# Performance work log

Hardware: AMD Instinct MI355X
Metric: run time of the kernel (lower is better)

The kernel has to match this reference:

```python
import jax, jax.numpy as jnp
import numpy as np

B, T, E, H = 8, 1024, 128, 8
S = E // H  # 16, narrow per-head dim


def setup_inputs() -> dict:
    key = jax.random.key(0)
    ks = jax.random.split(key, 7)
    return {
        "x": jax.random.normal(ks[0], (B, T, E), dtype=jnp.float32),
        "masks": jax.random.randint(ks[1], (B, T), 0, 2, dtype=jnp.int32),
        "Wq": jax.random.normal(ks[2], (S, S), dtype=jnp.float32) * 0.05,
        "Wk": jax.random.normal(ks[3], (S, S), dtype=jnp.float32) * 0.05,
        "Wv": jax.random.normal(ks[4], (S, S), dtype=jnp.float32) * 0.05,
        "Wu": jax.random.normal(ks[5], (E, E), dtype=jnp.float32) * 0.05,
        "bu": jnp.zeros((E,), dtype=jnp.float32),
        "temporal_only": 1,
    }


def reference(x, masks, Wq, Wk, Wv, Wu, bu, temporal_only):
    b, t, e = x.shape
    h = H
    s = e // h
    x4 = x.reshape(b, t, h, s)
    # nn.Linear(s, s, bias=False): y = x @ W.T, applied per head
    q = jnp.einsum('bths,ds->bthd', x4, Wq)
    k = jnp.einsum('bths,ds->bthd', x4, Wk)
    v = jnp.einsum('bths,ds->bthd', x4, Wv)
    scale = jnp.float32(e) ** 0.25
    q = q / scale
    k = k / scale
    # (b, h, t, t) attention logits
    dot = jnp.einsum('bqhd,bkhd->bhqk', q, k)
    # temporal_only masking: masks is (b, t), applied on key axis then query axis
    m = masks.astype(bool)
    neg = jnp.float32(-1e9)
    dot = jnp.where(m[:, None, None, :], dot, neg)
    dot = jnp.where(m[:, None, :, None], dot, neg)
    attn = jax.nn.softmax(dot, axis=-1)
    # post-softmax zeroing with the same masks
    attn = jnp.where(m[:, None, None, :], attn, jnp.float32(0.0))
    attn = jnp.where(m[:, None, :, None], attn, jnp.float32(0.0))
    out = jnp.einsum('bhqk,bkhd->bqhd', attn, v).reshape(b, t, h * s)
    return out @ Wu.T + bu
```

## Files before the change

### kernel.cpp

```cpp
#include <hip/hip_runtime.h>

#define NB 8
#define NT 1024
#define NE 128
#define NH 8
#define NS 16

#define WS_Q 0
#define WS_KC 1048576
#define WS_VC 2097152
#define WS_Y 3145728
#define WS_L 4194304
#define WS_VCNT (4194304 + 65536)

#define WT_PITCH 132

typedef float v2f __attribute__((ext_vector_type(2)));

static __device__ __forceinline__ v2f vlo(const float4 v) { return v2f{v.x, v.y}; }
static __device__ __forceinline__ v2f vhi(const float4 v) { return v2f{v.z, v.w}; }
static __device__ __forceinline__ v2f pfma(v2f a, v2f b, v2f c) {
  return __builtin_elementwise_fma(a, b, c);
}

static __device__ __forceinline__ float fexp2(float x) {
  return __builtin_amdgcn_exp2f(x);
}

static __device__ __forceinline__ void fma4(float4& acc, float s, const float4 v) {
  v2f lo = pfma(v2f{s, s}, vlo(v), vlo(acc));
  v2f hi = pfma(v2f{s, s}, vhi(v), vhi(acc));
  acc.x = lo.x; acc.y = lo.y; acc.z = hi.x; acc.w = hi.y;
}

static __device__ __forceinline__ float dot16p(const float4 q0, const float4 q1,
                                               const float4 q2, const float4 q3,
                                               const float4 k0, const float4 k1,
                                               const float4 k2, const float4 k3) {
  v2f a = vlo(q0) * vlo(k0);
  v2f b = vhi(q0) * vhi(k0);
  a = pfma(vlo(q1), vlo(k1), a);
  b = pfma(vhi(q1), vhi(k1), b);
  a = pfma(vlo(q2), vlo(k2), a);
  b = pfma(vhi(q2), vhi(k2), b);
  a = pfma(vlo(q3), vlo(k3), a);
  b = pfma(vhi(q3), vhi(k3), b);
  v2f c = a + b;
  return c.x + c.y;
}

__global__ __launch_bounds__(256) void qkv_kernel(
    const float* __restrict__ x, const int* __restrict__ masks,
    const float* __restrict__ Wq, const float* __restrict__ Wk,
    const float* __restrict__ Wv, float* __restrict__ Q,
    float* __restrict__ Kc, float* __restrict__ Vc, float* __restrict__ Y,
    float* __restrict__ L, int* __restrict__ vcount) {
  __shared__ __align__(16) float xs[64 * 20];
  __shared__ int posl[64];
  const int tid = threadIdx.x;
  const int h = blockIdx.x & 7;
  const int rg = blockIdx.x >> 3;
  const int b = rg >> 4;
  const int bt = (rg & 15) << 6;
  {
    const int sr = tid >> 2, sq = tid & 3;
    float4 xv =
        *(const float4*)(x + (size_t)(b * NT + bt + sr) * 128 + h * 16 + sq * 4);
    *(float4*)(xs + sr * 20 + sq * 4) = xv;
    *(float4*)(Y + (size_t)(b * NT + bt + sr) * NE + h * NS + sq * 4) =
        float4{0, 0, 0, 0};
  }
  if (tid < 64) {
    L[(size_t)(b * NH + h) * NT + bt + tid] = 0.f;
    int cnt = 0;
    for (int c = 0; c < bt; c += 64)
      cnt += __popcll(__ballot(masks[b * NT + c + tid] != 0));
    int v = masks[b * NT + bt + tid] != 0;
    unsigned long long bal = __ballot(v);
    posl[tid] = v ? (cnt + __popcll(bal & ((1ull << tid) - 1ull))) : -1;
    if (bt == NT - 64 && tid == 0) vcount[b] = cnt + __popcll(bal);
  }
  const int d = tid & 15;
  const int r = (tid >> 4) << 2;
  const float4* wq4 = (const float4*)(Wq + d * 16);
  const float4 wq0 = wq4[0], wq1 = wq4[1], wq2 = wq4[2], wq3 = wq4[3];
  const float4* wk4 = (const float4*)(Wk + d * 16);
  const float4 wk0 = wk4[0], wk1 = wk4[1], wk2 = wk4[2], wk3 = wk4[3];
  const float4* wv4 = (const float4*)(Wv + d * 16);
  const float4 wv0 = wv4[0], wv1 = wv4[1], wv2 = wv4[2], wv3 = wv4[3];
  const float invs = 0.12751744448143132f;
  __syncthreads();
#pragma unroll
  for (int i = 0; i < 4; i++) {
    const int row = r + i;
    const float4* xp = (const float4*)(xs + row * 20);
    const float4 x0 = xp[0], x1 = xp[1], x2 = xp[2], x3 = xp[3];
    float aq = dot16p(x0, x1, x2, x3, wq0, wq1, wq2, wq3);
    float ak = dot16p(x0, x1, x2, x3, wk0, wk1, wk2, wk3);
    float av = dot16p(x0, x1, x2, x3, wv0, wv1, wv2, wv3);
    const int t = bt + row;
    Q[((size_t)(b * NH + h) * NT + t) * NS + d] = aq * invs;
    const int pp = posl[row];
    if (pp >= 0) {
      size_t oc = ((size_t)(b * NH + h) * NT + pp) * NS + d;
      Kc[oc] = ak;
      Vc[oc] = av;
    }
  }
}

__global__ __launch_bounds__(512, 2) void attn_kernel(
    const float* __restrict__ Q, const float* __restrict__ Kc,
    const float* __restrict__ Vc, const int* __restrict__ vcount,
    float* __restrict__ Y, float* __restrict__ L) {
  __shared__ __align__(16) float smem[8192];
  float* Ks = smem;
  float* Vs = smem + 4096;
  const int tid = threadIdx.x;
  const int lane = tid & 63;
  const int s = tid >> 6;
  const int kh = blockIdx.x >> 8;
  const int rest = blockIdx.x & 255;
  const int bh = rest & 63;
  const int qg = rest >> 6;
  const int b = bh >> 3, h = bh & 7;
  const int tbase = qg << 8;
  const int nv = vcount[b];
  const int h0 = nv >> 1;
  const int kstart = kh ? h0 : 0;
  const int kend = kh ? nv : h0;

  float4 q[4][4];
#pragma unroll
  for (int qq = 0; qq < 4; qq++) {
    const float4* qg4 =
        (const float4*)(Q + ((size_t)bh * NT + tbase + (qq << 6) + lane) * NS);
    q[qq][0] = qg4[0]; q[qq][1] = qg4[1]; q[qq][2] = qg4[2]; q[qq][3] = qg4[3];
  }
  v2f o[4][8];
  float l[4];
#pragma unroll
  for (int qq = 0; qq < 4; qq++) {
    l[qq] = 0.f;
#pragma unroll
    for (int k = 0; k < 8; k++) o[qq][k] = v2f{0.f, 0.f};
  }

  const int quad = tid & 3;
  const int jr = tid >> 2;

#pragma unroll 1
  for (int k0 = kstart; k0 < kend; k0 += 256) {
    const int chunk = (kend - k0 < 256) ? (kend - k0) : 256;
    __syncthreads();
#pragma unroll
    for (int p = 0; p < 2; p++) {
      const int row = jr + (p << 7);
      float4 kv = {0, 0, 0, 0};
      if (row < chunk)
        kv = *(const float4*)(Kc + ((size_t)bh * NT + (k0 + row)) * NS +
                              (quad << 2));
      *(float4*)(Ks + row * 16 + (quad << 2)) = kv;
    }
#pragma unroll
    for (int p = 0; p < 2; p++) {
      const int row = jr + (p << 7);
      float4 vv = {0, 0, 0, 0};
      if (row < chunk)
        vv = *(const float4*)(Vc + ((size_t)bh * NT + (k0 + row)) * NS +
                              (quad << 2));
      *(float4*)(Vs + row * 16 + (quad << 2)) = vv;
    }
    __syncthreads();
#pragma unroll 2
    for (int g = 0; g < 8; g++) {
      const int rb = s + (g << 5);
      if (rb >= chunk) break;
      float sc[4][4];
#pragma unroll
      for (int i = 0; i < 4; i++) {
        const float4* kr = (const float4*)(Ks + (rb + (i << 3)) * 16);
        const float4 k0v = kr[0], k1v = kr[1], k2v = kr[2], k3v = kr[3];
#pragma unroll
        for (int qq = 0; qq < 4; qq++)
          sc[qq][i] =
              dot16p(q[qq][0], q[qq][1], q[qq][2], q[qq][3], k0v, k1v, k2v, k3v);
      }
#pragma unroll
      for (int i = 0; i < 4; i++)
        if (rb + (i << 3) >= chunk) {
          sc[0][i] = -1e30f; sc[1][i] = -1e30f;
          sc[2][i] = -1e30f; sc[3][i] = -1e30f;
        }
      float p[4][4];
#pragma unroll
      for (int qq = 0; qq < 4; qq++) {
        p[qq][0] = fexp2(sc[qq][0]);
        p[qq][1] = fexp2(sc[qq][1]);
        p[qq][2] = fexp2(sc[qq][2]);
        p[qq][3] = fexp2(sc[qq][3]);
        l[qq] += (p[qq][0] + p[qq][1]) + (p[qq][2] + p[qq][3]);
      }
#pragma unroll
      for (int i = 0; i < 4; i++) {
        const float4* vr = (const float4*)(Vs + (rb + (i << 3)) * 16);
        const float4 v0 = vr[0], v1 = vr[1], v2 = vr[2], v3 = vr[3];
#pragma unroll
        for (int qq = 0; qq < 4; qq++) {
          const v2f pq = {p[qq][i], p[qq][i]};
          o[qq][0] = pfma(pq, vlo(v0), o[qq][0]);
          o[qq][1] = pfma(pq, vhi(v0), o[qq][1]);
          o[qq][2] = pfma(pq, vlo(v1), o[qq][2]);
          o[qq][3] = pfma(pq, vhi(v1), o[qq][3]);
          o[qq][4] = pfma(pq, vlo(v2), o[qq][4]);
          o[qq][5] = pfma(pq, vhi(v2), o[qq][5]);
          o[qq][6] = pfma(pq, vlo(v3), o[qq][6]);
          o[qq][7] = pfma(pq, vhi(v3), o[qq][7]);
        }
      }
    }
  }

  float* om = smem;
  const int q8 = tid >> 3;
  const int sub = tid & 7;
#pragma unroll
  for (int ph = 0; ph < 4; ph++) {
    v2f ysum = {0.f, 0.f};
    float Lsum = 0.f;
    __syncthreads();
    if (s < 4) {
      float* pa = om + (s * 64 + lane) * 20;
#pragma unroll
      for (int k = 0; k < 8; k++) *(v2f*)(pa + k * 2) = o[ph][k];
      pa[16] = l[ph];
    }
    __syncthreads();
#pragma unroll
    for (int ss = 0; ss < 4; ss++) {
      const float* pp = om + (ss * 64 + q8) * 20;
      Lsum += pp[16];
      ysum += *(const v2f*)(pp + sub * 2);
    }
    __syncthreads();
    if (s >= 4) {
      float* pa = om + ((s - 4) * 64 + lane) * 20;
#pragma unroll
      for (int k = 0; k < 8; k++) *(v2f*)(pa + k * 2) = o[ph][k];
      pa[16] = l[ph];
    }
    __syncthreads();
#pragma unroll
    for (int ss = 0; ss < 4; ss++) {
      const float* pp = om + (ss * 64 + q8) * 20;
      Lsum += pp[16];
      ysum += *(const v2f*)(pp + sub * 2);
    }
    const int tq = tbase + (ph << 6) + q8;
    float* yp = Y + ((size_t)b * NT + tq) * NE + h * NS + sub * 2;
    atomicAdd(yp + 0, ysum.x);
    atomicAdd(yp + 1, ysum.y);
    if (sub == 0) atomicAdd(L + (size_t)bh * NT + tq, Lsum);
  }
}

__global__ __launch_bounds__(256) void proj_kernel(
    const float* __restrict__ Y, const float* __restrict__ L,
    const int* __restrict__ masks, const float* __restrict__ Wu,
    const float* __restrict__ bu, float* __restrict__ out) {
  __shared__ __align__(16) float Wt[64 * WT_PITCH];
  __shared__ __align__(16) float Yt[16 * 128];
  const int tid = threadIdx.x;
  const int r0 = blockIdx.x * 16;
  const int bb = r0 >> 10;
  const float4* yg = (const float4*)(Y + (size_t)r0 * 128);
  float4* yt4 = (float4*)Yt;
  {
#pragma unroll
    for (int p = 0; p < 2; p++) {
      const int idx = tid + p * 256;
      const int row = idx >> 5;
      const int head = (idx & 31) >> 2;
      const int t = (r0 + row) & 1023;
      const float Lv = L[(size_t)(bb * NH + head) * NT + t];
      const int qm = masks[r0 + row];
      const float inv = (qm != 0 && Lv > 0.f) ? (1.0f / Lv) : 0.f;
      float4 v = yg[idx];
      v.x *= inv; v.y *= inv; v.z *= inv; v.w *= inv;
      yt4[idx] = v;
    }
  }
  const int c0 = (tid & 31) << 2;
  const int rg = (tid >> 5) & 3;
  const int eh = tid >> 7;
  float4 acc0 = {0, 0, 0, 0}, acc1 = {0, 0, 0, 0}, acc2 = {0, 0, 0, 0},
         acc3 = {0, 0, 0, 0};
  for (int e0 = 0; e0 < 128; e0 += 64) {
    __syncthreads();
#pragma unroll
    for (int p = 0; p < 8; p++) {
      int idx = tid + p * 256;
      int c = idx >> 4;
      int es = (idx & 15) << 2;
      float4 w = *(const float4*)(Wu + c * 128 + e0 + es);
      Wt[(es + 0) * WT_PITCH + c] = w.x;
      Wt[(es + 1) * WT_PITCH + c] = w.y;
      Wt[(es + 2) * WT_PITCH + c] = w.z;
      Wt[(es + 3) * WT_PITCH + c] = w.w;
    }
    __syncthreads();
    const int eb = eh << 5;
    const float* y0 = Yt + (rg * 4 + 0) * 128 + e0 + eb;
    const float* y1 = Yt + (rg * 4 + 1) * 128 + e0 + eb;
    const float* y2 = Yt + (rg * 4 + 2) * 128 + e0 + eb;
    const float* y3 = Yt + (rg * 4 + 3) * 128 + e0 + eb;
#pragma unroll 4
    for (int e = 0; e < 32; e += 4) {
      const float* wb = Wt + (eb + e) * WT_PITCH + c0;
      float4 w0 = *(const float4*)(wb + 0 * WT_PITCH);
      float4 w1 = *(const float4*)(wb + 1 * WT_PITCH);
      float4 w2 = *(const float4*)(wb + 2 * WT_PITCH);
      float4 w3 = *(const float4*)(wb + 3 * WT_PITCH);
      float4 ya = *(const float4*)(y0 + e);
      float4 yb = *(const float4*)(y1 + e);
      float4 yc = *(const float4*)(y2 + e);
      float4 yd = *(const float4*)(y3 + e);
      fma4(acc0, ya.x, w0); fma4(acc0, ya.y, w1); fma4(acc0, ya.z, w2); fma4(acc0, ya.w, w3);
      fma4(acc1, yb.x, w0); fma4(acc1, yb.y, w1); fma4(acc1, yb.z, w2); fma4(acc1, yb.w, w3);
      fma4(acc2, yc.x, w0); fma4(acc2, yc.y, w1); fma4(acc2, yc.z, w2); fma4(acc2, yc.w, w3);
      fma4(acc3, yd.x, w0); fma4(acc3, yd.y, w1); fma4(acc3, yd.z, w2); fma4(acc3, yd.w, w3);
    }
  }
  __syncthreads();
  if (eh == 1) {
    float* p = Wt + (tid & 127) * 20;
    *(float4*)(p + 0) = acc0; *(float4*)(p + 4) = acc1;
    *(float4*)(p + 8) = acc2; *(float4*)(p + 12) = acc3;
  }
  __syncthreads();
  if (eh == 0) {
    const float* p = Wt + tid * 20;
    float4 b4 = *(const float4*)(bu + c0);
    float4 q0 = *(const float4*)(p + 0);
    float4 q1 = *(const float4*)(p + 4);
    float4 q2 = *(const float4*)(p + 8);
    float4 q3 = *(const float4*)(p + 12);
    acc0.x += q0.x + b4.x; acc0.y += q0.y + b4.y; acc0.z += q0.z + b4.z; acc0.w += q0.w + b4.w;
    acc1.x += q1.x + b4.x; acc1.y += q1.y + b4.y; acc1.z += q1.z + b4.z; acc1.w += q1.w + b4.w;
    acc2.x += q2.x + b4.x; acc2.y += q2.y + b4.y; acc2.z += q2.z + b4.z; acc2.w += q2.w + b4.w;
    acc3.x += q3.x + b4.x; acc3.y += q3.y + b4.y; acc3.z += q3.z + b4.z; acc3.w += q3.w + b4.w;
    *(float4*)(out + (size_t)(r0 + rg * 4 + 0) * 128 + c0) = acc0;
    *(float4*)(out + (size_t)(r0 + rg * 4 + 1) * 128 + c0) = acc1;
    *(float4*)(out + (size_t)(r0 + rg * 4 + 2) * 128 + c0) = acc2;
    *(float4*)(out + (size_t)(r0 + rg * 4 + 3) * 128 + c0) = acc3;
  }
}

extern "C" void kernel_launch(void* const* d_in, const int* in_sizes, int n_in,
                              void* d_out, int out_size, void* d_ws,
                              size_t ws_size, hipStream_t stream) {
  const float* x = (const float*)d_in[0];
  const int* masks = (const int*)d_in[1];
  const float* Wq = (const float*)d_in[2];
  const float* Wk = (const float*)d_in[3];
  const float* Wv = (const float*)d_in[4];
  const float* Wu = (const float*)d_in[5];
  const float* bu = (const float*)d_in[6];
  float* out = (float*)d_out;

  float* ws = (float*)d_ws;
  float* Q = ws + WS_Q;
  float* Kc = ws + WS_KC;
  float* Vc = ws + WS_VC;
  float* Y = ws + WS_Y;
  float* L = ws + WS_L;
  int* vcount = (int*)(ws + WS_VCNT);

  qkv_kernel<<<1024, 256, 0, stream>>>(x, masks, Wq, Wk, Wv, Q, Kc, Vc, Y, L,
                                       vcount);
  attn_kernel<<<2 * 4 * NB * NH, 512, 0, stream>>>(Q, Kc, Vc, vcount, Y, L);
  proj_kernel<<<NB * NT / 16, 256, 0, stream>>>(Y, L, masks, Wu, bu, out);
}
```

Before: 136.7 us.

## Replace atomic split-K accumulation with per-half partial buffers summed in projection

Each of the two key-split attention blocks now writes its partial output and row-sum into its own buffer with plain stores, and the projection kernel adds the two halves before normalising. This removes the float atomics, the zero-initialisation of Y and L in the QKV kernel, and two of the four barriers per phase in the in-block reduction, since all eight waves now write to a larger shared buffer at once. In exchange it uses more workspace, more shared memory per block (40 KB instead of 32 KB), and an extra global read of the second buffer in the projection kernel.

```diff
diff --git a/kernel.cpp b/kernel.cpp
--- a/kernel.cpp
+++ b/kernel.cpp
@@ -9,9 +9,11 @@
 #define WS_Q 0
 #define WS_KC 1048576
 #define WS_VC 2097152
-#define WS_Y 3145728
-#define WS_L 4194304
-#define WS_VCNT (4194304 + 65536)
+#define WS_Y0 3145728
+#define WS_Y1 4194304
+#define WS_L0 5242880
+#define WS_L1 (5242880 + 65536)
+#define WS_VCNT (5242880 + 131072)
 
 #define WT_PITCH 132
 
@@ -53,8 +55,7 @@
     const float* __restrict__ x, const int* __restrict__ masks,
     const float* __restrict__ Wq, const float* __restrict__ Wk,
     const float* __restrict__ Wv, float* __restrict__ Q,
-    float* __restrict__ Kc, float* __restrict__ Vc, float* __restrict__ Y,
-    float* __restrict__ L, int* __restrict__ vcount) {
+    float* __restrict__ Kc, float* __restrict__ Vc, int* __restrict__ vcount) {
   __shared__ __align__(16) float xs[64 * 20];
   __shared__ int posl[64];
   const int tid = threadIdx.x;
@@ -67,11 +68,8 @@
     float4 xv =
         *(const float4*)(x + (size_t)(b * NT + bt + sr) * 128 + h * 16 + sq * 4);
     *(float4*)(xs + sr * 20 + sq * 4) = xv;
-    *(float4*)(Y + (size_t)(b * NT + bt + sr) * NE + h * NS + sq * 4) =
-        float4{0, 0, 0, 0};
   }
   if (tid < 64) {
-    L[(size_t)(b * NH + h) * NT + bt + tid] = 0.f;
     int cnt = 0;
     for (int c = 0; c < bt; c += 64)
       cnt += __popcll(__ballot(masks[b * NT + c + tid] != 0));
@@ -112,8 +110,9 @@
 __global__ __launch_bounds__(512, 2) void attn_kernel(
     const float* __restrict__ Q, const float* __restrict__ Kc,
     const float* __restrict__ Vc, const int* __restrict__ vcount,
-    float* __restrict__ Y, float* __restrict__ L) {
-  __shared__ __align__(16) float smem[8192];
+    float* __restrict__ Y0, float* __restrict__ Y1, float* __restrict__ L0,
+    float* __restrict__ L1) {
+  __shared__ __align__(16) float smem[10240];
   float* Ks = smem;
   float* Vs = smem + 4096;
   const int tid = threadIdx.x;
@@ -129,6 +128,8 @@
   const int h0 = nv >> 1;
   const int kstart = kh ? h0 : 0;
   const int kend = kh ? nv : h0;
+  float* Yh = kh ? Y1 : Y0;
+  float* Lh = kh ? L1 : L0;
 
   float4 q[4][4];
 #pragma unroll
@@ -226,46 +227,33 @@
   const int sub = tid & 7;
 #pragma unroll
   for (int ph = 0; ph < 4; ph++) {
-    v2f ysum = {0.f, 0.f};
-    float Lsum = 0.f;
-    __syncthreads();
-    if (s < 4) {
+    __syncthreads();
+    {
       float* pa = om + (s * 64 + lane) * 20;
 #pragma unroll
       for (int k = 0; k < 8; k++) *(v2f*)(pa + k * 2) = o[ph][k];
       pa[16] = l[ph];
     }
     __syncthreads();
-#pragma unroll
-    for (int ss = 0; ss < 4; ss++) {
-      const float* pp = om + (ss * 64 + q8) * 20;
-      Lsum += pp[16];
-      ysum += *(const v2f*)(pp + sub * 2);
-    }
-    __syncthreads();
-    if (s >= 4) {
-      float* pa = om + ((s - 4) * 64 + lane) * 20;
-#pragma unroll
-      for (int k = 0; k < 8; k++) *(v2f*)(pa + k * 2) = o[ph][k];
-      pa[16] = l[ph];
-    }
-    __syncthreads();
-#pragma unroll
-    for (int ss = 0; ss < 4; ss++) {
-      const float* pp = om + (ss * 64 + q8) * 20;
-      Lsum += pp[16];
-      ysum += *(const v2f*)(pp + sub * 2);
-    }
-    const int tq = tbase + (ph << 6) + q8;
-    float* yp = Y + ((size_t)b * NT + tq) * NE + h * NS + sub * 2;
-    atomicAdd(yp + 0, ysum.x);
-    atomicAdd(yp + 1, ysum.y);
-    if (sub == 0) atomicAdd(L + (size_t)bh * NT + tq, Lsum);
+    {
+      float Lsum = 0.f;
+      v2f ysum = {0.f, 0.f};
+#pragma unroll
+      for (int ss = 0; ss < 8; ss++) {
+        const float* pp = om + (ss * 64 + q8) * 20;
+        Lsum += pp[16];
+        ysum += *(const v2f*)(pp + sub * 2);
+      }
+      const int tq = tbase + (ph << 6) + q8;
+      *(v2f*)(Yh + ((size_t)b * NT + tq) * NE + h * NS + sub * 2) = ysum;
+      if (sub == 0) Lh[(size_t)bh * NT + tq] = Lsum;
+    }
   }
 }
 
 __global__ __launch_bounds__(256) void proj_kernel(
-    const float* __restrict__ Y, const float* __restrict__ L,
+    const float* __restrict__ Y0, const float* __restrict__ Y1,
+    const float* __restrict__ L0, const float* __restrict__ L1,
     const int* __restrict__ masks, const float* __restrict__ Wu,
     const float* __restrict__ bu, float* __restrict__ out) {
   __shared__ __align__(16) float Wt[64 * WT_PITCH];
@@ -273,7 +261,8 @@
   const int tid = threadIdx.x;
   const int r0 = blockIdx.x * 16;
   const int bb = r0 >> 10;
-  const float4* yg = (const float4*)(Y + (size_t)r0 * 128);
+  const float4* yg0 = (const float4*)(Y0 + (size_t)r0 * 128);
+  const float4* yg1 = (const float4*)(Y1 + (size_t)r0 * 128);
   float4* yt4 = (float4*)Yt;
   {
 #pragma unroll
@@ -282,12 +271,15 @@
       const int row = idx >> 5;
       const int head = (idx & 31) >> 2;
       const int t = (r0 + row) & 1023;
-      const float Lv = L[(size_t)(bb * NH + head) * NT + t];
+      const size_t li = (size_t)(bb * NH + head) * NT + t;
+      const float Lv = L0[li] + L1[li];
       const int qm = masks[r0 + row];
       const float inv = (qm != 0 && Lv > 0.f) ? (1.0f / Lv) : 0.f;
-      float4 v = yg[idx];
-      v.x *= inv; v.y *= inv; v.z *= inv; v.w *= inv;
-      yt4[idx] = v;
+      float4 a = yg0[idx];
+      float4 c = yg1[idx];
+      a.x = (a.x + c.x) * inv; a.y = (a.y + c.y) * inv;
+      a.z = (a.z + c.z) * inv; a.w = (a.w + c.w) * inv;
+      yt4[idx] = a;
     }
   }
   const int c0 = (tid & 31) << 2;
@@ -372,12 +364,16 @@
   float* Q = ws + WS_Q;
   float* Kc = ws + WS_KC;
   float* Vc = ws + WS_VC;
-  float* Y = ws + WS_Y;
-  float* L = ws + WS_L;
+  float* Y0 = ws + WS_Y0;
+  float* Y1 = ws + WS_Y1;
+  float* L0 = ws + WS_L0;
+  float* L1 = ws + WS_L1;
   int* vcount = (int*)(ws + WS_VCNT);
 
-  qkv_kernel<<<1024, 256, 0, stream>>>(x, masks, Wq, Wk, Wv, Q, Kc, Vc, Y, L,
+  qkv_kernel<<<1024, 256, 0, stream>>>(x, masks, Wq, Wk, Wv, Q, Kc, Vc,
                                        vcount);
-  attn_kernel<<<2 * 4 * NB * NH, 512, 0, stream>>>(Q, Kc, Vc, vcount, Y, L);
-  proj_kernel<<<NB * NT / 16, 256, 0, stream>>>(Y, L, masks, Wu, bu, out);
-}
+  attn_kernel<<<2 * 4 * NB * NH, 512, 0, stream>>>(Q, Kc, Vc, vcount, Y0, Y1,
+                                                   L0, L1);
+  proj_kernel<<<NB * NT / 16, 256, 0, stream>>>(Y0, Y1, L0, L1, masks, Wu, bu,
+                                                out);
+}
```

After: 133.6 us. 2.3% less time.
